# Kernel optimization log

Measured on AMD Instinct MI355X. Metric: run time of the kernel, lower is better.

## Reference

```python
import jax, jax.numpy as jnp
import numpy as np

B, K, C, HEADS, R, N, FF = 8, 512, 256, 8, 4, 64, 1024
HT = 2 * R + 1  # rel-pos table side = 9


def layer_norm(x, g, b, eps=1e-5):
    mu = jnp.mean(x, axis=-1, keepdims=True)
    var = jnp.var(x, axis=-1, keepdims=True)
    return (x - mu) * jax.lax.rsqrt(var + eps) * g + b


def grid_sample_table(table, grid):
    """Bilinear grid_sample, align_corners=True, zeros padding.
    table: [heads, H, W] (batch-expanded in torch, identical per batch)
    grid:  [b, k, n, 2] in [-1, 1]  ->  out [b, heads, k, n]
    """
    heads, H, W = table.shape
    gx = (grid[..., 0] + 1.0) * 0.5 * (W - 1)
    gy = (grid[..., 1] + 1.0) * 0.5 * (H - 1)
    x0 = jnp.floor(gx); y0 = jnp.floor(gy)
    x1 = x0 + 1.0;      y1 = y0 + 1.0
    wx1 = gx - x0; wx0 = 1.0 - wx1
    wy1 = gy - y0; wy0 = 1.0 - wy1
    flat = table.reshape(heads, H * W)

    def corner(yi, xi, w):
        valid = (xi >= 0) & (xi <= W - 1) & (yi >= 0) & (yi <= H - 1)
        idx = (jnp.clip(yi, 0, H - 1) * W + jnp.clip(xi, 0, W - 1)).astype(jnp.int32)
        return flat[:, idx] * jnp.where(valid, w, 0.0)[None]  # [heads,b,k,n]

    out = (corner(y0, x0, wy0 * wx0) + corner(y0, x1, wy0 * wx1)
           + corner(y1, x0, wy1 * wx0) + corner(y1, x1, wy1 * wx1))
    return jnp.moveaxis(out, 0, 1)  # [b, heads, k, n]


def setup_inputs() -> dict:
    key = jax.random.key(0)
    ks = jax.random.split(key, 16)
    s = 1.0 / np.sqrt(C)
    inp = {
        "query": jax.random.normal(ks[0], (B, K, C), jnp.float32),
        "local_feat": jax.random.normal(ks[1], (B, C, K, N), jnp.float32),
        "local_spat": jax.random.uniform(ks[2], (B, K, N, 2), jnp.float32) * 2.0 - 1.0,
        # rel-pos table is zeros-initialized in torch; use small randn so it's non-trivial
        "rel_table": jax.random.normal(ks[3], (HEADS, HT, HT), jnp.float32) * 0.02,
        "Wq": jax.random.normal(ks[4], (C, C), jnp.float32) * s,
        "bq": jnp.zeros((C,), jnp.float32),
        "Wk": jax.random.normal(ks[5], (C, C), jnp.float32) * s,
        "bk": jnp.zeros((C,), jnp.float32),
        "Wv": jax.random.normal(ks[6], (C, C), jnp.float32) * s,
        "bv": jnp.zeros((C,), jnp.float32),
        "Wo": jax.random.normal(ks[7], (C, C), jnp.float32) * s,
        "bo": jnp.zeros((C,), jnp.float32),
        "ln1_g": jnp.ones((C,), jnp.float32),
        "ln1_b": jnp.zeros((C,), jnp.float32),
        "W1": jax.random.normal(ks[8], (C, FF), jnp.float32) * s,
        "b1": jnp.zeros((FF,), jnp.float32),
        "W2": jax.random.normal(ks[9], (FF, C), jnp.float32) * (1.0 / np.sqrt(FF)),
        "b2": jnp.zeros((C,), jnp.float32),
        "ln2_g": jnp.ones((C,), jnp.float32),
        "ln2_b": jnp.zeros((C,), jnp.float32),
    }
    return inp


def reference(query, local_feat, local_spat, rel_table, Wq, bq, Wk, bk, Wv, bv,
              Wo, bo, ln1_g, ln1_b, W1, b1, W2, b2, ln2_g, ln2_b):
    b, k, c = query.shape
    heads = rel_table.shape[0]
    d = c // heads
    n = local_feat.shape[-1]
    # spatial_score: grid_sample of rel-pos table at per-key offsets -> attention bias
    bias = grid_sample_table(rel_table, local_spat)      # [b, heads, k, n]
    bias = jnp.transpose(bias, (0, 2, 1, 3))             # [b, k, heads, n]
    # local bilateral attention (query attends to its n local samples)
    q = (query @ Wq + bq).reshape(b, k, heads, d)
    feats = jnp.transpose(local_feat, (0, 2, 3, 1))      # [b, k, n, c]
    Kp = (feats @ Wk + bk).reshape(b, k, n, heads, d)
    Vp = (feats @ Wv + bv).reshape(b, k, n, heads, d)
    scores = jnp.einsum('bkhd,bknhd->bkhn', q, Kp) / jnp.sqrt(jnp.float32(d)) + bias
    attn = jax.nn.softmax(scores, axis=-1)
    ctx = jnp.einsum('bkhn,bknhd->bkhd', attn, Vp).reshape(b, k, c)
    x = layer_norm(query + ctx @ Wo + bo, ln1_g, ln1_b)
    h = jax.nn.gelu(x @ W1 + b1) @ W2 + b2
    out = layer_norm(x + h, ln2_g, ln2_b)
    # num_local_scales == 1: stack+mean over scales is identity
    return out
```

## Files before the change

kernel.cpp:

```cpp
#include <hip/hip_runtime.h>
#include <hip/hip_bf16.h>

typedef __hip_bfloat16 bf16;
typedef __attribute__((ext_vector_type(8))) short short8;
typedef __attribute__((ext_vector_type(4))) float float4_;

#define DEV static __device__ __forceinline__

DEV float blo(unsigned w){ return __uint_as_float(w << 16); }
DEV float bhi(unsigned w){ return __uint_as_float(w & 0xffff0000u); }
DEV unsigned short f2bu(float x){ bf16 h = __float2bfloat16(x); unsigned short u; __builtin_memcpy(&u, &h, 2); return u; }
DEV unsigned pack2(float a, float b){ return (unsigned)f2bu(a) | ((unsigned)f2bu(b) << 16); }

DEV float gelu_tanh(float x){
  float z = 0.7978845608028654f * (x + 0.044715f * x * x * x);
  float th = 2.0f / (1.0f + __expf(-2.0f * z)) - 1.0f;
  return 0.5f * x * (1.0f + th);
}


__global__ __launch_bounds__(256) void k_prep(
    const float* __restrict__ query, const float* __restrict__ Wq,
    const float* __restrict__ Wk, const float* __restrict__ Wv,
    const float* __restrict__ Wo, const float* __restrict__ W1, const float* __restrict__ W2,
    bf16* __restrict__ query_bf, bf16* __restrict__ WqT, bf16* __restrict__ WkP,
    bf16* __restrict__ WvP, bf16* __restrict__ WoT, bf16* __restrict__ W1T, bf16* __restrict__ W2T)
{
  const size_t stride = (size_t)gridDim.x * 256;
  for (size_t i = (size_t)blockIdx.x * 256 + threadIdx.x; i < 1048576; i += stride){
    query_bf[i] = __float2bfloat16(query[i]);
    if (i < 262144){
      { int n = i >> 8,  k = i & 255;  W1T[i] = __float2bfloat16(W1[(size_t)k*1024 + n]); }
      { int n = i >> 10, k = i & 1023; W2T[i] = __float2bfloat16(W2[(size_t)k*256 + n]); }
    }
    if (i < 65536){
      { int n = i >> 8, k = i & 255; WqT[i] = __float2bfloat16(Wq[(size_t)k*256 + n]);
                                     WoT[i] = __float2bfloat16(Wo[(size_t)k*256 + n]); }
      { int h = i >> 13, c = (i >> 5) & 255, d = i & 31;
        WkP[i] = __float2bfloat16(Wk[(size_t)c*256 + h*32 + d]); }
      { int h = i >> 13, d = (i >> 8) & 31, c = i & 255;
        WvP[i] = __float2bfloat16(Wv[(size_t)c*256 + h*32 + d]); }
    }
  }
}

template<int KDIM, int NT, int EPI>
__global__ __launch_bounds__(256) void k_gemm(
    const bf16* __restrict__ A, int lda, int acolH,
    const bf16* __restrict__ BT, int btH,
    const float* __restrict__ bias,
    const float* __restrict__ resid, int ldr,
    float* __restrict__ Cf, bf16* __restrict__ Cb, int ldc, int ncolH)
{
  constexpr int KB = (KDIM >= 64) ? 64 : 32;
  constexpr int LP = KB + 8;
  constexpr int ASEG = KB / 8;
  __shared__ short As[64][LP];
  __shared__ short Bs[NT][LP];

  const int t = threadIdx.x;
  const int w = t >> 6, l = t & 63, lm = l & 15, lq = l >> 4;
  const int m0 = blockIdx.x * 64;
  const int h = blockIdx.z;
  const size_t acol = (size_t)h * acolH;
  const bf16* Bt = BT + (size_t)h * btH + (size_t)(blockIdx.y * NT) * KDIM;
  const int ncol = h * ncolH + blockIdx.y * NT;

  float4_ acc[NT/16];
  #pragma unroll
  for (int i = 0; i < NT/16; i++) acc[i] = (float4_){0.f,0.f,0.f,0.f};

  for (int k0 = 0; k0 < KDIM; k0 += KB){
    if (k0) __syncthreads();
    for (int i = t; i < 64*ASEG; i += 256){
      int row = i / ASEG, seg = i % ASEG;
      uint4 v = *(const uint4*)(A + (size_t)(m0+row)*lda + acol + k0 + seg*8);
      *(uint4*)&As[row][seg*8] = v;
    }
    for (int i = t; i < NT*ASEG; i += 256){
      int row = i / ASEG, seg = i % ASEG;
      uint4 v = *(const uint4*)(Bt + (size_t)row*KDIM + k0 + seg*8);
      *(uint4*)&Bs[row][seg*8] = v;
    }
    __syncthreads();
    #pragma unroll
    for (int kk = 0; kk < KB/32; kk++){
      short8 af = *(const short8*)&As[w*16 + lm][kk*32 + lq*8];
      #pragma unroll
      for (int nt = 0; nt < NT/16; nt++){
        short8 bfr = *(const short8*)&Bs[nt*16 + lm][kk*32 + lq*8];
        acc[nt] = __builtin_amdgcn_mfma_f32_16x16x32_bf16(af, bfr, acc[nt], 0, 0, 0);
      }
    }
  }

  #pragma unroll
  for (int nt = 0; nt < NT/16; nt++){
    int gcol = ncol + nt*16 + lm;
    float bb = bias ? bias[gcol] : 0.0f;
    #pragma unroll
    for (int rg = 0; rg < 4; rg++){
      int row = m0 + w*16 + lq*4 + rg;
      float v = acc[nt][rg] + bb;
      if (EPI == 0)      Cb[(size_t)row*ldc + gcol] = __float2bfloat16(v);
      else if (EPI == 1) Cf[(size_t)row*ldc + gcol] = v + resid[(size_t)row*ldr + gcol];
      else               Cb[(size_t)row*ldc + gcol] = __float2bfloat16(gelu_tanh(v));
    }
  }
}

__global__ __launch_bounds__(256) void k_attn(
    const float* __restrict__ local_feat, const float* __restrict__ local_spat,
    const float* __restrict__ rel_table, const bf16* __restrict__ qk,
    bf16* __restrict__ fctx)
{
  __shared__ ushort fs[256][66];
  __shared__ float qks[8][256];
  __shared__ float sc[8][64];
  __shared__ float attn_t[64][8];
  __shared__ float tab[648];
  __shared__ float bw4[64][4];
  __shared__ int   bix[64][4];

  const int t = threadIdx.x;
  const int r = blockIdx.x;
  const int b = r >> 9, k = r & 511;

  {
    int cb = t >> 2;
    int nq = (t & 3) * 16;
    #pragma unroll
    for (int p = 0; p < 4; p++){
      int c = p * 64 + cb;
      const float4* src = (const float4*)(local_feat + ((size_t)((b*256 + c)*512 + k))*64 + nq);
      unsigned* d = (unsigned*)&fs[c][nq];
      #pragma unroll
      for (int g = 0; g < 4; g++){
        float4 v = src[g];
        d[g*2+0] = pack2(v.x, v.y);
        d[g*2+1] = pack2(v.z, v.w);
      }
    }
  }
  {
    const uint4* src = (const uint4*)(qk + (size_t)r * 2048 + t * 8);
    uint4 a = *src;
    int h = t >> 5, c0 = (t & 31) * 8;
    float* d = &qks[h][c0];
    d[0]=blo(a.x); d[1]=bhi(a.x); d[2]=blo(a.y); d[3]=bhi(a.y);
    d[4]=blo(a.z); d[5]=bhi(a.z); d[6]=blo(a.w); d[7]=bhi(a.w);
  }
  for (int i = t; i < 648; i += 256) tab[i] = rel_table[i];
  if (t < 64){
    int n = t;
    float2 sxy = *(const float2*)&local_spat[((size_t)r*64 + n)*2];
    float gx = (sxy.x + 1.0f) * 4.0f, gy = (sxy.y + 1.0f) * 4.0f;
    float x0f = floorf(gx), y0f = floorf(gy);
    int xi0 = (int)x0f, yi0 = (int)y0f;
    float wx1 = gx - x0f, wx0 = 1.0f - wx1;
    float wy1 = gy - y0f, wy0 = 1.0f - wy1;
    int xs[4] = {xi0, xi0 + 1, xi0, xi0 + 1};
    int ys[4] = {yi0, yi0, yi0 + 1, yi0 + 1};
    float ww[4] = {wy0*wx0, wy0*wx1, wy1*wx0, wy1*wx1};
    #pragma unroll
    for (int j2 = 0; j2 < 4; j2++){
      int xx = xs[j2], yy = ys[j2];
      bool valid = (xx >= 0) && (xx <= 8) && (yy >= 0) && (yy <= 8);
      int xc = min(max(xx, 0), 8), yc = min(max(yy, 0), 8);
      bix[n][j2] = yc * 9 + xc;
      bw4[n][j2] = valid ? ww[j2] : 0.0f;
    }
  }
  __syncthreads();

  {
    int h = t >> 5, n0 = (t & 31) * 2;
    float s0 = 0.f, s1 = 0.f;
    for (int c = 0; c < 256; c += 4){
      float4 qv = *(const float4*)&qks[h][c];
      unsigned w0 = *(const unsigned*)&fs[c+0][n0];
      unsigned w1 = *(const unsigned*)&fs[c+1][n0];
      unsigned w2 = *(const unsigned*)&fs[c+2][n0];
      unsigned w3 = *(const unsigned*)&fs[c+3][n0];
      s0 += qv.x*blo(w0) + qv.y*blo(w1) + qv.z*blo(w2) + qv.w*blo(w3);
      s1 += qv.x*bhi(w0) + qv.y*bhi(w1) + qv.z*bhi(w2) + qv.w*bhi(w3);
    }
    const float scale = 0.17677669529663687f;
    float bias0 = tab[h*81 + bix[n0][0]] * bw4[n0][0] + tab[h*81 + bix[n0][1]] * bw4[n0][1]
                + tab[h*81 + bix[n0][2]] * bw4[n0][2] + tab[h*81 + bix[n0][3]] * bw4[n0][3];
    int n1 = n0 + 1;
    float bias1 = tab[h*81 + bix[n1][0]] * bw4[n1][0] + tab[h*81 + bix[n1][1]] * bw4[n1][1]
                + tab[h*81 + bix[n1][2]] * bw4[n1][2] + tab[h*81 + bix[n1][3]] * bw4[n1][3];
    sc[h][n0] = s0 * scale + bias0;
    sc[h][n1] = s1 * scale + bias1;
  }
  __syncthreads();

  if (t < 8){
    int h = t;
    float m = -1e30f;
    for (int n = 0; n < 64; n++) m = fmaxf(m, sc[h][n]);
    float s = 0.f;
    for (int n = 0; n < 64; n++){ float e = __expf(sc[h][n] - m); sc[h][n] = e; s += e; }
    float inv = 1.0f / s;
    for (int n = 0; n < 64; n++) attn_t[n][h] = sc[h][n] * inv;
  }
  __syncthreads();

  {
    const int c = t;
    float f[8] = {0,0,0,0,0,0,0,0};
    for (int n = 0; n < 64; n += 2){
      unsigned wa = *(const unsigned*)&fs[c][n];
      float a0 = blo(wa), a1 = bhi(wa);
      float4 A0 = *(const float4*)&attn_t[n][0];
      float4 A1 = *(const float4*)&attn_t[n][4];
      float4 B0 = *(const float4*)&attn_t[n+1][0];
      float4 B1 = *(const float4*)&attn_t[n+1][4];
      f[0] += A0.x*a0 + B0.x*a1;  f[1] += A0.y*a0 + B0.y*a1;
      f[2] += A0.z*a0 + B0.z*a1;  f[3] += A0.w*a0 + B0.w*a1;
      f[4] += A1.x*a0 + B1.x*a1;  f[5] += A1.y*a0 + B1.y*a1;
      f[6] += A1.z*a0 + B1.z*a1;  f[7] += A1.w*a0 + B1.w*a1;
    }
    #pragma unroll
    for (int h = 0; h < 8; h++)
      fctx[(size_t)r*2048 + h*256 + c] = __float2bfloat16(f[h]);
  }
}

__global__ __launch_bounds__(256) void k_ln(const float* __restrict__ in,
    const float* __restrict__ g, const float* __restrict__ bb,
    float* __restrict__ out, bf16* __restrict__ out_bf)
{
  __shared__ float w1[4], w2[4];
  const int t = threadIdx.x, r = blockIdx.x;
  float v = in[(size_t)r*256 + t];
  float s1 = v, s2 = v*v;
  #pragma unroll
  for (int o = 32; o > 0; o >>= 1){ s1 += __shfl_down(s1, o); s2 += __shfl_down(s2, o); }
  if ((t & 63) == 0){ w1[t >> 6] = s1; w2[t >> 6] = s2; }
  __syncthreads();
  if (t == 0){
    float a = w1[0] + w1[1] + w1[2] + w1[3];
    float bs = w2[0] + w2[1] + w2[2] + w2[3];
    float mean = a * (1.0f/256.0f);
    float var = bs * (1.0f/256.0f) - mean*mean;
    w1[0] = mean; w2[0] = rsqrtf(var + 1e-5f);
  }
  __syncthreads();
  float mean = w1[0], inv = w2[0];
  float o = (v - mean) * inv * g[t] + bb[t];
  out[(size_t)r*256 + t] = o;
  if (out_bf) out_bf[(size_t)r*256 + t] = __float2bfloat16(o);
}

extern "C" void kernel_launch(void* const* d_in, const int* in_sizes, int n_in,
                              void* d_out, int out_size, void* d_ws, size_t ws_size,
                              hipStream_t stream)
{
  const float* query      = (const float*)d_in[0];
  const float* local_feat = (const float*)d_in[1];
  const float* local_spat = (const float*)d_in[2];
  const float* rel_table  = (const float*)d_in[3];
  const float* Wq  = (const float*)d_in[4];   const float* bq  = (const float*)d_in[5];
  const float* Wk  = (const float*)d_in[6];
  const float* Wv  = (const float*)d_in[8];   const float* bv  = (const float*)d_in[9];
  const float* Wo  = (const float*)d_in[10];  const float* bo  = (const float*)d_in[11];
  const float* g1  = (const float*)d_in[12];  const float* be1 = (const float*)d_in[13];
  const float* W1  = (const float*)d_in[14];  const float* b1  = (const float*)d_in[15];
  const float* W2  = (const float*)d_in[16];  const float* b2  = (const float*)d_in[17];
  const float* g2  = (const float*)d_in[18];  const float* be2 = (const float*)d_in[19];

  char* ws = (char*)d_ws;
  bf16*  qk       = (bf16*)(ws + 0);
  bf16*  fctx     = (bf16*)(ws + 16777216);
  bf16*  query_bf = (bf16*)(ws + 33554432);
  bf16*  q_bf     = (bf16*)(ws + 35651584);
  bf16*  WqT      = (bf16*)(ws + 37748736);
  bf16*  WkP      = (bf16*)(ws + 37879808);
  bf16*  WvP      = (bf16*)(ws + 38010880);
  bf16*  WoT      = (bf16*)(ws + 38141952);
  bf16*  W1T      = (bf16*)(ws + 38273024);
  bf16*  W2T      = (bf16*)(ws + 38797312);
  bf16*  ctx_bf   = (bf16*)(ws + 0);
  float* ao       = (float*)(ws + 2097152);
  float* y        = (float*)(ws + 6291456);
  bf16*  x_bf     = (bf16*)(ws + 10485760);
  float* x        = (float*)(ws + 16777216);
  bf16*  h1       = (bf16*)(ws + 20971520);
  float* out      = (float*)d_out;

  dim3 blk(256);
  k_prep<<<dim3(1024), blk, 0, stream>>>(query, Wq, Wk, Wv, Wo, W1, W2,
                                         query_bf, WqT, WkP, WvP, WoT, W1T, W2T);
  k_gemm<256,64,0><<<dim3(64,4,1), blk, 0, stream>>>(query_bf, 256, 0, WqT, 0, bq,
                                                     nullptr, 0, nullptr, q_bf, 256, 0);
  k_gemm<32,64,0><<<dim3(64,4,8), blk, 0, stream>>>(q_bf, 256, 32, WkP, 8192, nullptr,
                                                    nullptr, 0, nullptr, qk, 2048, 256);
  k_attn<<<dim3(4096), blk, 0, stream>>>(local_feat, local_spat, rel_table, qk, fctx);
  k_gemm<256,32,0><<<dim3(64,1,8), blk, 0, stream>>>(fctx, 2048, 256, WvP, 8192, bv,
                                                     nullptr, 0, nullptr, ctx_bf, 256, 32);
  k_gemm<256,64,1><<<dim3(64,4,1), blk, 0, stream>>>(ctx_bf, 256, 0, WoT, 0, bo,
                                                     query, 256, ao, nullptr, 256, 0);
  k_ln<<<dim3(4096), blk, 0, stream>>>(ao, g1, be1, x, x_bf);
  k_gemm<256,64,2><<<dim3(64,16,1), blk, 0, stream>>>(x_bf, 256, 0, W1T, 0, b1,
                                                      nullptr, 0, nullptr, h1, 1024, 0);
  k_gemm<1024,64,1><<<dim3(64,4,1), blk, 0, stream>>>(h1, 1024, 0, W2T, 0, b2,
                                                      x, 256, y, nullptr, 256, 0);
  k_ln<<<dim3(4096), blk, 0, stream>>>(y, g2, be2, out, nullptr);
}
```

Measured before the change: 533.5 us.

## Fuse residual+LayerNorm into GEMM epilogues, tile weight prep, warp-level softmax

Adds a k_gemm_ln kernel in which each block computes 16 full 256-wide rows, so the residual add and LayerNorm run in the GEMM epilogue. This removes two k_ln launches and the fp32 intermediate round trips. k_prep now transposes weights through shared-memory tiles with vectorized loads and stores, instead of strided scalar reads over a 1024-block grid. The attention softmax moves from an 8-thread serial loop to per-warp shuffle reductions. The cost is that the full-row GEMM uses only 256 blocks, each loading the whole 256-row B tile per k-step, which may lower parallelism for the K=1024 GEMM.

```diff
diff --git a/kernel.cpp b/kernel.cpp
--- a/kernel.cpp
+++ b/kernel.cpp
@@ -26,20 +26,74 @@
     bf16* __restrict__ query_bf, bf16* __restrict__ WqT, bf16* __restrict__ WkP,
     bf16* __restrict__ WvP, bf16* __restrict__ WoT, bf16* __restrict__ W1T, bf16* __restrict__ W2T)
 {
-  const size_t stride = (size_t)gridDim.x * 256;
-  for (size_t i = (size_t)blockIdx.x * 256 + threadIdx.x; i < 1048576; i += stride){
-    query_bf[i] = __float2bfloat16(query[i]);
-    if (i < 262144){
-      { int n = i >> 8,  k = i & 255;  W1T[i] = __float2bfloat16(W1[(size_t)k*1024 + n]); }
-      { int n = i >> 10, k = i & 1023; W2T[i] = __float2bfloat16(W2[(size_t)k*256 + n]); }
-    }
-    if (i < 65536){
-      { int n = i >> 8, k = i & 255; WqT[i] = __float2bfloat16(Wq[(size_t)k*256 + n]);
-                                     WoT[i] = __float2bfloat16(Wo[(size_t)k*256 + n]); }
-      { int h = i >> 13, c = (i >> 5) & 255, d = i & 31;
-        WkP[i] = __float2bfloat16(Wk[(size_t)c*256 + h*32 + d]); }
-      { int h = i >> 13, d = (i >> 8) & 31, c = i & 255;
-        WvP[i] = __float2bfloat16(Wv[(size_t)c*256 + h*32 + d]); }
+  __shared__ ushort ts[64][72];
+  const int t = threadIdx.x;
+  const int bx = blockIdx.x;
+
+  if (bx < 160){
+    const float* src; bf16* dst; int ldi, ldo, kt, nt;
+    if (bx < 16)      { src = Wq; dst = WqT; ldi = 256;  ldo = 256;  kt = bx & 3;        nt = bx >> 2; }
+    else if (bx < 32) { src = Wo; dst = WoT; ldi = 256;  ldo = 256;  kt = (bx-16) & 3;   nt = (bx-16) >> 2; }
+    else if (bx < 96) { src = W1; dst = W1T; ldi = 1024; ldo = 256;  kt = (bx-32) & 3;   nt = (bx-32) >> 2; }
+    else              { src = W2; dst = W2T; ldi = 256;  ldo = 1024; kt = (bx-96) & 15;  nt = (bx-96) >> 4; }
+    int k0 = kt * 64, n0 = nt * 64;
+    {
+      int r = t >> 2, c0 = (t & 3) * 16;
+      #pragma unroll
+      for (int g = 0; g < 4; g++){
+        float4 v = *(const float4*)&src[(size_t)(k0 + r)*ldi + n0 + c0 + g*4];
+        ts[r][c0+g*4+0] = f2bu(v.x); ts[r][c0+g*4+1] = f2bu(v.y);
+        ts[r][c0+g*4+2] = f2bu(v.z); ts[r][c0+g*4+3] = f2bu(v.w);
+      }
+    }
+    __syncthreads();
+    {
+      int rr = t >> 2, cc0 = (t & 3) * 16;
+      unsigned wbuf[8];
+      #pragma unroll
+      for (int j = 0; j < 8; j++)
+        wbuf[j] = (unsigned)ts[cc0+2*j][rr] | ((unsigned)ts[cc0+2*j+1][rr] << 16);
+      uint4* d = (uint4*)(dst + (size_t)(n0 + rr)*ldo + k0 + cc0);
+      d[0] = make_uint4(wbuf[0], wbuf[1], wbuf[2], wbuf[3]);
+      d[1] = make_uint4(wbuf[4], wbuf[5], wbuf[6], wbuf[7]);
+    }
+  } else if (bx < 192){
+    int idx = bx - 160, h = idx >> 2, kt = idx & 3, k0 = kt * 64;
+    {
+      int r = t >> 2, d0 = (t & 3) * 8;
+      #pragma unroll
+      for (int g = 0; g < 2; g++){
+        float4 v = *(const float4*)&Wv[(size_t)(k0 + r)*256 + h*32 + d0 + g*4];
+        ts[r][d0+g*4+0] = f2bu(v.x); ts[r][d0+g*4+1] = f2bu(v.y);
+        ts[r][d0+g*4+2] = f2bu(v.z); ts[r][d0+g*4+3] = f2bu(v.w);
+      }
+    }
+    __syncthreads();
+    {
+      int d = t >> 3, cc0 = (t & 7) * 8;
+      unsigned wbuf[4];
+      #pragma unroll
+      for (int j = 0; j < 4; j++)
+        wbuf[j] = (unsigned)ts[cc0+2*j][d] | ((unsigned)ts[cc0+2*j+1][d] << 16);
+      *(uint4*)(WvP + (size_t)h*8192 + (size_t)d*256 + k0 + cc0) =
+          make_uint4(wbuf[0], wbuf[1], wbuf[2], wbuf[3]);
+    }
+  } else if (bx < 200){
+    int off = (bx - 192) * 8192;
+    #pragma unroll
+    for (int g = 0; g < 8; g++){
+      int i = off + g*1024 + t*4;
+      int h = i >> 13, c = (i >> 5) & 255, d = i & 31;
+      float4 v = *(const float4*)&Wk[(size_t)c*256 + h*32 + d];
+      *(uint2*)(WkP + i) = make_uint2(pack2(v.x, v.y), pack2(v.z, v.w));
+    }
+  } else {
+    int off = (bx - 200) * 16384;
+    #pragma unroll
+    for (int g = 0; g < 16; g++){
+      int i = off + g*1024 + t*4;
+      float4 v = *(const float4*)&query[i];
+      *(uint2*)(query_bf + i) = make_uint2(pack2(v.x, v.y), pack2(v.z, v.w));
     }
   }
 }
@@ -49,8 +103,7 @@
     const bf16* __restrict__ A, int lda, int acolH,
     const bf16* __restrict__ BT, int btH,
     const float* __restrict__ bias,
-    const float* __restrict__ resid, int ldr,
-    float* __restrict__ Cf, bf16* __restrict__ Cb, int ldc, int ncolH)
+    bf16* __restrict__ Cb, int ldc, int ncolH)
 {
   constexpr int KB = (KDIM >= 64) ? 64 : 32;
   constexpr int LP = KB + 8;
@@ -102,9 +155,101 @@
     for (int rg = 0; rg < 4; rg++){
       int row = m0 + w*16 + lq*4 + rg;
       float v = acc[nt][rg] + bb;
-      if (EPI == 0)      Cb[(size_t)row*ldc + gcol] = __float2bfloat16(v);
-      else if (EPI == 1) Cf[(size_t)row*ldc + gcol] = v + resid[(size_t)row*ldr + gcol];
-      else               Cb[(size_t)row*ldc + gcol] = __float2bfloat16(gelu_tanh(v));
+      if (EPI == 0) Cb[(size_t)row*ldc + gcol] = __float2bfloat16(v);
+      else          Cb[(size_t)row*ldc + gcol] = __float2bfloat16(gelu_tanh(v));
+    }
+  }
+}
+
+template<int KDIM, int WRITE_BF>
+__global__ __launch_bounds__(256) void k_gemm_ln(
+    const bf16* __restrict__ A, int lda,
+    const bf16* __restrict__ BT,
+    const float* __restrict__ bias,
+    const float* __restrict__ resid,
+    const float* __restrict__ gamma, const float* __restrict__ beta,
+    float* __restrict__ Cf, bf16* __restrict__ Cb)
+{
+  constexpr int KB = 64, LP = 72;
+  __shared__ short As[16][LP];
+  __shared__ short Bs[256][LP];
+  __shared__ float2 part[4][16];
+
+  const int t = threadIdx.x;
+  const int w = t >> 6, l = t & 63, lm = l & 15, lq = l >> 4;
+  const int m0 = blockIdx.x * 16;
+
+  float4_ acc[4];
+  #pragma unroll
+  for (int i = 0; i < 4; i++) acc[i] = (float4_){0.f,0.f,0.f,0.f};
+
+  for (int k0 = 0; k0 < KDIM; k0 += KB){
+    if (k0) __syncthreads();
+    if (t < 128){
+      int row = t >> 3, seg = t & 7;
+      uint4 v = *(const uint4*)(A + (size_t)(m0+row)*lda + k0 + seg*8);
+      *(uint4*)&As[row][seg*8] = v;
+    }
+    for (int i = t; i < 2048; i += 256){
+      int row = i >> 3, seg = i & 7;
+      uint4 v = *(const uint4*)(BT + (size_t)row*KDIM + k0 + seg*8);
+      *(uint4*)&Bs[row][seg*8] = v;
+    }
+    __syncthreads();
+    #pragma unroll
+    for (int kk = 0; kk < 2; kk++){
+      short8 af = *(const short8*)&As[lm][kk*32 + lq*8];
+      #pragma unroll
+      for (int nt = 0; nt < 4; nt++){
+        short8 bfr = *(const short8*)&Bs[w*64 + nt*16 + lm][kk*32 + lq*8];
+        acc[nt] = __builtin_amdgcn_mfma_f32_16x16x32_bf16(af, bfr, acc[nt], 0, 0, 0);
+      }
+    }
+  }
+
+  float v[4][4];
+  float s1[4] = {0,0,0,0}, s2[4] = {0,0,0,0};
+  #pragma unroll
+  for (int nt = 0; nt < 4; nt++){
+    int col = w*64 + nt*16 + lm;
+    float bb = bias[col];
+    #pragma unroll
+    for (int rg = 0; rg < 4; rg++){
+      int row = m0 + lq*4 + rg;
+      float x = acc[nt][rg] + bb + resid[(size_t)row*256 + col];
+      v[nt][rg] = x;
+      s1[rg] += x; s2[rg] += x*x;
+    }
+  }
+  #pragma unroll
+  for (int off = 1; off < 16; off <<= 1){
+    #pragma unroll
+    for (int rg = 0; rg < 4; rg++){
+      s1[rg] += __shfl_xor(s1[rg], off);
+      s2[rg] += __shfl_xor(s2[rg], off);
+    }
+  }
+  if (lm == 0){
+    #pragma unroll
+    for (int rg = 0; rg < 4; rg++)
+      part[w][lq*4 + rg] = make_float2(s1[rg], s2[rg]);
+  }
+  __syncthreads();
+  #pragma unroll
+  for (int rg = 0; rg < 4; rg++){
+    int rl = lq*4 + rg;
+    float S1 = part[0][rl].x + part[1][rl].x + part[2][rl].x + part[3][rl].x;
+    float S2 = part[0][rl].y + part[1][rl].y + part[2][rl].y + part[3][rl].y;
+    float mean = S1 * (1.0f/256.0f);
+    float var  = S2 * (1.0f/256.0f) - mean*mean;
+    float inv  = rsqrtf(var + 1e-5f);
+    #pragma unroll
+    for (int nt = 0; nt < 4; nt++){
+      int col = w*64 + nt*16 + lm;
+      float o = (v[nt][rg] - mean) * inv * gamma[col] + beta[col];
+      size_t idx = (size_t)(m0 + rl)*256 + col;
+      Cf[idx] = o;
+      if (WRITE_BF) Cb[idx] = __float2bfloat16(o);
     }
   }
 }
@@ -116,8 +261,7 @@
 {
   __shared__ ushort fs[256][66];
   __shared__ float qks[8][256];
-  __shared__ float sc[8][64];
-  __shared__ float attn_t[64][8];
+  __shared__ float attn_t[64][12];
   __shared__ float tab[648];
   __shared__ float bw4[64][4];
   __shared__ int   bix[64][4];
@@ -186,24 +330,23 @@
       s1 += qv.x*bhi(w0) + qv.y*bhi(w1) + qv.z*bhi(w2) + qv.w*bhi(w3);
     }
     const float scale = 0.17677669529663687f;
+    int n1 = n0 + 1;
     float bias0 = tab[h*81 + bix[n0][0]] * bw4[n0][0] + tab[h*81 + bix[n0][1]] * bw4[n0][1]
                 + tab[h*81 + bix[n0][2]] * bw4[n0][2] + tab[h*81 + bix[n0][3]] * bw4[n0][3];
-    int n1 = n0 + 1;
     float bias1 = tab[h*81 + bix[n1][0]] * bw4[n1][0] + tab[h*81 + bix[n1][1]] * bw4[n1][1]
                 + tab[h*81 + bix[n1][2]] * bw4[n1][2] + tab[h*81 + bix[n1][3]] * bw4[n1][3];
-    sc[h][n0] = s0 * scale + bias0;
-    sc[h][n1] = s1 * scale + bias1;
-  }
-  __syncthreads();
-
-  if (t < 8){
-    int h = t;
-    float m = -1e30f;
-    for (int n = 0; n < 64; n++) m = fmaxf(m, sc[h][n]);
-    float s = 0.f;
-    for (int n = 0; n < 64; n++){ float e = __expf(sc[h][n] - m); sc[h][n] = e; s += e; }
+    float sc0 = s0 * scale + bias0;
+    float sc1 = s1 * scale + bias1;
+    float m = fmaxf(sc0, sc1);
+    #pragma unroll
+    for (int off = 1; off < 32; off <<= 1) m = fmaxf(m, __shfl_xor(m, off));
+    float e0 = __expf(sc0 - m), e1 = __expf(sc1 - m);
+    float s = e0 + e1;
+    #pragma unroll
+    for (int off = 1; off < 32; off <<= 1) s += __shfl_xor(s, off);
     float inv = 1.0f / s;
-    for (int n = 0; n < 64; n++) attn_t[n][h] = sc[h][n] * inv;
+    attn_t[n0][h] = e0 * inv;
+    attn_t[n1][h] = e1 * inv;
   }
   __syncthreads();
 
@@ -226,32 +369,6 @@
     for (int h = 0; h < 8; h++)
       fctx[(size_t)r*2048 + h*256 + c] = __float2bfloat16(f[h]);
   }
-}
-
-__global__ __launch_bounds__(256) void k_ln(const float* __restrict__ in,
-    const float* __restrict__ g, const float* __restrict__ bb,
-    float* __restrict__ out, bf16* __restrict__ out_bf)
-{
-  __shared__ float w1[4], w2[4];
-  const int t = threadIdx.x, r = blockIdx.x;
-  float v = in[(size_t)r*256 + t];
-  float s1 = v, s2 = v*v;
-  #pragma unroll
-  for (int o = 32; o > 0; o >>= 1){ s1 += __shfl_down(s1, o); s2 += __shfl_down(s2, o); }
-  if ((t & 63) == 0){ w1[t >> 6] = s1; w2[t >> 6] = s2; }
-  __syncthreads();
-  if (t == 0){
-    float a = w1[0] + w1[1] + w1[2] + w1[3];
-    float bs = w2[0] + w2[1] + w2[2] + w2[3];
-    float mean = a * (1.0f/256.0f);
-    float var = bs * (1.0f/256.0f) - mean*mean;
-    w1[0] = mean; w2[0] = rsqrtf(var + 1e-5f);
-  }
-  __syncthreads();
-  float mean = w1[0], inv = w2[0];
-  float o = (v - mean) * inv * g[t] + bb[t];
-  out[(size_t)r*256 + t] = o;
-  if (out_bf) out_bf[(size_t)r*256 + t] = __float2bfloat16(o);
 }
 
 extern "C" void kernel_launch(void* const* d_in, const int* in_sizes, int n_in,
@@ -283,29 +400,19 @@
   bf16*  W1T      = (bf16*)(ws + 38273024);
   bf16*  W2T      = (bf16*)(ws + 38797312);
   bf16*  ctx_bf   = (bf16*)(ws + 0);
-  float* ao       = (float*)(ws + 2097152);
-  float* y        = (float*)(ws + 6291456);
-  bf16*  x_bf     = (bf16*)(ws + 10485760);
-  float* x        = (float*)(ws + 16777216);
+  float* x        = (float*)(ws + 2097152);
+  bf16*  x_bf     = (bf16*)(ws + 6291456);
   bf16*  h1       = (bf16*)(ws + 20971520);
   float* out      = (float*)d_out;
 
   dim3 blk(256);
-  k_prep<<<dim3(1024), blk, 0, stream>>>(query, Wq, Wk, Wv, Wo, W1, W2,
-                                         query_bf, WqT, WkP, WvP, WoT, W1T, W2T);
-  k_gemm<256,64,0><<<dim3(64,4,1), blk, 0, stream>>>(query_bf, 256, 0, WqT, 0, bq,
-                                                     nullptr, 0, nullptr, q_bf, 256, 0);
-  k_gemm<32,64,0><<<dim3(64,4,8), blk, 0, stream>>>(q_bf, 256, 32, WkP, 8192, nullptr,
-                                                    nullptr, 0, nullptr, qk, 2048, 256);
+  k_prep<<<dim3(264), blk, 0, stream>>>(query, Wq, Wk, Wv, Wo, W1, W2,
+                                        query_bf, WqT, WkP, WvP, WoT, W1T, W2T);
+  k_gemm<256,64,0><<<dim3(64,4,1), blk, 0, stream>>>(query_bf, 256, 0, WqT, 0, bq, q_bf, 256, 0);
+  k_gemm<32,64,0><<<dim3(64,4,8), blk, 0, stream>>>(q_bf, 256, 32, WkP, 8192, nullptr, qk, 2048, 256);
   k_attn<<<dim3(4096), blk, 0, stream>>>(local_feat, local_spat, rel_table, qk, fctx);
-  k_gemm<256,32,0><<<dim3(64,1,8), blk, 0, stream>>>(fctx, 2048, 256, WvP, 8192, bv,
-                                                     nullptr, 0, nullptr, ctx_bf, 256, 32);
-  k_gemm<256,64,1><<<dim3(64,4,1), blk, 0, stream>>>(ctx_bf, 256, 0, WoT, 0, bo,
-                                                     query, 256, ao, nullptr, 256, 0);
-  k_ln<<<dim3(4096), blk, 0, stream>>>(ao, g1, be1, x, x_bf);
-  k_gemm<256,64,2><<<dim3(64,16,1), blk, 0, stream>>>(x_bf, 256, 0, W1T, 0, b1,
-                                                      nullptr, 0, nullptr, h1, 1024, 0);
-  k_gemm<1024,64,1><<<dim3(64,4,1), blk, 0, stream>>>(h1, 1024, 0, W2T, 0, b2,
-                                                      x, 256, y, nullptr, 256, 0);
-  k_ln<<<dim3(4096), blk, 0, stream>>>(y, g2, be2, out, nullptr);
-}
+  k_gemm<256,32,0><<<dim3(64,1,8), blk, 0, stream>>>(fctx, 2048, 256, WvP, 8192, bv, ctx_bf, 256, 32);
+  k_gemm_ln<256,1><<<dim3(256), blk, 0, stream>>>(ctx_bf, 256, WoT, bo, query, g1, be1, x, x_bf);
+  k_gemm<256,64,2><<<dim3(64,16,1), blk, 0, stream>>>(x_bf, 256, 0, W1T, 0, b1, h1, 1024, 0);
+  k_gemm_ln<1024,0><<<dim3(256), blk, 0, stream>>>(h1, 1024, W2T, b2, x, g2, be2, out, nullptr);
+}
```

After: 524.9 us. No clear change (-1.6%).
